# Optimization experiments

Measured on AMD Instinct MI355X. Metric: run time of the kernel, lower is better.

## Reference

```python
import jax, jax.numpy as jnp
import numpy as np

DIM = 192; D_STATE = 16; D_CONV = 4; EXPAND = 2
D_INNER = EXPAND * DIM          # 384
DT_RANK = -(-DIM // 16)         # ceil(192/16) = 12
BSZ, T, H, W = 1, 16, 64, 64


def setup_inputs() -> dict:
    key = jax.random.key(0)
    ks = jax.random.split(key, 10)
    s = 0.02
    return {
        "x": jax.random.normal(ks[0], (BSZ, DIM, T, H, W), jnp.float32),
        "ln1_g": jnp.ones((DIM,), jnp.float32),
        "ln1_b": jnp.zeros((DIM,), jnp.float32),
        "ln2_g": jnp.ones((DIM,), jnp.float32),
        "ln2_b": jnp.zeros((DIM,), jnp.float32),
        "W_in": jax.random.normal(ks[1], (2 * D_INNER, DIM), jnp.float32) * s,
        "conv_w": jax.random.normal(ks[2], (D_INNER, D_CONV), jnp.float32) * 0.3,
        "conv_b": jnp.zeros((D_INNER,), jnp.float32),
        "W_xp": jax.random.normal(ks[3], (DT_RANK + 2 * D_STATE, D_INNER), jnp.float32) * s,
        "W_dt": jax.random.normal(ks[4], (D_INNER, DT_RANK), jnp.float32) * 0.1,
        "b_dt": jax.random.normal(ks[5], (D_INNER,), jnp.float32) * 0.1 - 4.0,
        "A_log": jnp.log(jnp.broadcast_to(jnp.arange(1, D_STATE + 1, dtype=jnp.float32), (D_INNER, D_STATE))),
        "D": jnp.ones((D_INNER,), jnp.float32),
        "W_out": jax.random.normal(ks[6], (DIM, D_INNER), jnp.float32) * s,
    }


def _layer_norm(x, g, b, eps=1e-5):
    m = x.mean(-1, keepdims=True)
    v = ((x - m) ** 2).mean(-1, keepdims=True)
    return (x - m) * jax.lax.rsqrt(v + eps) * g + b


def _mamba(tokens, W_in, conv_w, conv_b, W_xp, W_dt, b_dt, A_log, D, W_out):
    B, L, _ = tokens.shape
    xz = tokens @ W_in.T                      # (B, L, 2*d_inner)
    xc, z = jnp.split(xz, 2, axis=-1)
    # causal depthwise conv1d along L
    xin = xc.transpose(0, 2, 1)               # (B, d_inner, L)
    xconv = jax.lax.conv_general_dilated(
        xin, conv_w[:, None, :], (1,), [(D_CONV - 1, 0)],
        dimension_numbers=("NCH", "OIH", "NCH"), feature_group_count=D_INNER)
    xconv = xconv + conv_b[None, :, None]
    xs = jax.nn.silu(xconv.transpose(0, 2, 1))  # (B, L, d_inner)
    x_dbl = xs @ W_xp.T                        # (B, L, dt_rank + 2*d_state)
    dt, Bm, Cm = jnp.split(x_dbl, [DT_RANK, DT_RANK + D_STATE], axis=-1)
    dt = jax.nn.softplus(dt @ W_dt.T + b_dt)   # (B, L, d_inner)
    A = -jnp.exp(A_log)                        # (d_inner, d_state)
    dA = jnp.exp(dt[..., None] * A)            # (B, L, d_inner, d_state)
    dBx = dt[..., None] * Bm[:, :, None, :] * xs[..., None]

    def step(h, inp):
        dA_t, dBx_t, C_t = inp
        h = dA_t * h + dBx_t                   # (B, d_inner, d_state)
        return h, jnp.einsum("bds,bs->bd", h, C_t)

    h0 = jnp.zeros((B, D_INNER, D_STATE), tokens.dtype)
    _, ys = jax.lax.scan(step, h0, (dA.transpose(1, 0, 2, 3),
                                    dBx.transpose(1, 0, 2, 3),
                                    Cm.transpose(1, 0, 2)))
    y = ys.transpose(1, 0, 2) + xs * D         # (B, L, d_inner)
    y = y * jax.nn.silu(z)
    return y @ W_out.T                          # (B, L, dim)


def reference(x, ln1_g, ln1_b, ln2_g, ln2_b, W_in, conv_w, conv_b,
              W_xp, W_dt, b_dt, A_log, D, W_out):
    B, C, T_, H_, W_ = x.shape
    Hs, Ws = H_ // 4, W_ // 4
    # avg_pool3d kernel=(1,4,4) stride=(1,4,4)
    x_ds = x.reshape(B, C, T_, Hs, 4, Ws, 4).mean((4, 6))
    tokens = x_ds.reshape(B, C, T_ * Hs * Ws).transpose(0, 2, 1)  # (B, L, C)
    y = _layer_norm(tokens, ln1_g, ln1_b)
    y = _mamba(y, W_in, conv_w, conv_b, W_xp, W_dt, b_dt, A_log, D, W_out)
    out = _layer_norm(tokens + y, ln2_g, ln2_b)                    # (B, L, C)
    out5 = out.transpose(0, 2, 1).reshape(B, C, T_, Hs, Ws)
    pooled = out5.mean((3, 4))                                     # (B, C, T)
    mag = jnp.abs(jnp.fft.rfft(pooled, axis=2))
    weight = jax.nn.sigmoid(mag[:, :, 1:8].mean(-1))               # (B, C)
    out5 = out5 * weight[:, :, None, None, None]
    up = jax.image.resize(out5, (B, C, T_, H_, W_), method="trilinear")
    return up * jax.nn.sigmoid(x)
```

## Files before the change

kernel.cpp:

```cpp
#include <hip/hip_runtime.h>
#include <math.h>

#define DIMC 192
#define DI   384
#define DS   16
#define LTOK 4096
#define NCH  128
#define CLEN 32
#define NLANE (DI*DS)
#define L2E  1.4426950408889634f
#define LN2  0.6931471805599453f

typedef __attribute__((ext_vector_type(8))) short    bf16x8;
typedef __attribute__((ext_vector_type(8))) unsigned short u16x8;
typedef __attribute__((ext_vector_type(4))) float    f32x4;

__device__ __forceinline__ float EXP2(float x) { return __builtin_amdgcn_exp2f(x); }
__device__ __forceinline__ float RCP(float x)  { return __builtin_amdgcn_rcpf(x); }
__device__ __forceinline__ float LOG2(float x) { return __builtin_amdgcn_logf(x); }

__device__ __forceinline__ float sigmoidf_(float x) { return RCP(1.f + EXP2(-x * L2E)); }
__device__ __forceinline__ float siluf_(float x)    { return x * RCP(1.f + EXP2(-x * L2E)); }
__device__ __forceinline__ unsigned short f2bf(float f) {
    unsigned int u = __float_as_uint(f);
    u += 0x7FFFu + ((u >> 16) & 1u);
    return (unsigned short)(u >> 16);
}
__device__ __forceinline__ float bf2f(unsigned short b) {
    return __uint_as_float(((unsigned int)b) << 16);
}

__global__ __launch_bounds__(256) void poolln_kernel(const float* __restrict__ x,
                                                     const float* __restrict__ g,
                                                     const float* __restrict__ bb,
                                                     const float* __restrict__ W_in,
                                                     const float* __restrict__ W_out,
                                                     const float* __restrict__ W_xp,
                                                     const float* __restrict__ A_log,
                                                     unsigned short* __restrict__ tokb,
                                                     unsigned short* __restrict__ ytok,
                                                     unsigned short* __restrict__ W_in_bf,
                                                     unsigned short* __restrict__ W_out_bf,
                                                     unsigned short* __restrict__ W_xp_pad,
                                                     float* __restrict__ A2pre,
                                                     float* __restrict__ pooled) {
    int blk = blockIdx.x;
    int tid = threadIdx.x;
    if (blk >= 256) {
        int id = (blk - 256) * 256 + tid;
        for (int i = id; i < 768 * 192; i += 8192) W_in_bf[i] = f2bf(W_in[i]);
        for (int i = id; i < 192 * 384; i += 8192) W_out_bf[i] = f2bf(W_out[i]);
        for (int i = id; i < 64 * 384; i += 8192) {
            int row = i / 384;
            W_xp_pad[i] = (row < 44) ? f2bf(W_xp[i]) : (unsigned short)0;
        }
        for (int i = id; i < NLANE; i += 8192) A2pre[i] = -expf(A_log[i]) * L2E;
        for (int i = id; i < 192 * 16; i += 8192) pooled[i] = 0.f;
        return;
    }
    int t = blk >> 4, hs = blk & 15;
    int grp = tid >> 4, ws = tid & 15;
    __shared__ float P[16 * 196];
    __shared__ float ms[16], rs[16];
    #pragma unroll
    for (int k = 0; k < 12; ++k) {
        int c = grp + (k << 4);
        const float* base = x + ((size_t)(c * 16 + t) * 64 + hs * 4) * 64 + ws * 4;
        float s = 0.f;
        #pragma unroll
        for (int i = 0; i < 4; ++i) {
            float4 v = *(const float4*)(base + i * 64);
            s += v.x + v.y + v.z + v.w;
        }
        P[ws * 196 + c] = s * 0.0625f;
    }
    __syncthreads();
    float s1 = 0.f, s2 = 0.f;
    #pragma unroll
    for (int k = 0; k < 12; ++k) {
        float v = P[grp * 196 + ws + 16 * k];
        s1 += v; s2 += v * v;
    }
    s1 += __shfl_xor(s1, 1); s2 += __shfl_xor(s2, 1);
    s1 += __shfl_xor(s1, 2); s2 += __shfl_xor(s2, 2);
    s1 += __shfl_xor(s1, 4); s2 += __shfl_xor(s2, 4);
    s1 += __shfl_xor(s1, 8); s2 += __shfl_xor(s2, 8);
    if (ws == 0) {
        float m = s1 * (1.f / 192.f);
        ms[grp] = m;
        rs[grp] = rsqrtf(s2 * (1.f / 192.f) - m * m + 1e-5f);
    }
    __syncthreads();
    int l0 = t * 256 + hs * 16;
    for (int e = tid; e < 16 * 192; e += 256) {
        int w2 = e / 192, c = e - w2 * 192;
        float v = P[w2 * 196 + c];
        float val = (v - ms[w2]) * rs[w2] * g[c] + bb[c];
        tokb[(size_t)(l0 + w2) * DIMC + c] = f2bf(v);
        ytok[(size_t)(l0 + w2) * DIMC + c] = f2bf(val);
    }
}

__global__ __launch_bounds__(256) void gemm_in(const unsigned short* __restrict__ A,
                                               const unsigned short* __restrict__ Wb,
                                               unsigned short* __restrict__ xcb,
                                               unsigned short* __restrict__ zsb) {
    constexpr int K = 192, KP = K + 8;
    __shared__ unsigned short As[64 * KP];
    __shared__ unsigned short Bs[64 * KP];
    int bm = blockIdx.y * 64;
    int bn = blockIdx.x * 64;
    int tid = threadIdx.x;
    int lane = tid & 63, w = tid >> 6;
    int wr = w >> 1, wc = w & 1;
    int r16 = lane & 15, h = lane >> 4;
    for (int c = tid; c < 64 * (K / 8); c += 256) {
        int row = c / (K / 8), col = (c % (K / 8)) * 8;
        *(u16x8*)&As[row * KP + col] = *(const u16x8*)(A + (size_t)(bm + row) * K + col);
        *(u16x8*)&Bs[row * KP + col] = *(const u16x8*)(Wb + (size_t)(bn + row) * K + col);
    }
    __syncthreads();
    f32x4 acc[2][2] = {};
    #pragma unroll
    for (int k0 = 0; k0 < K; k0 += 32) {
        bf16x8 a0 = *(const bf16x8*)&As[(wr * 32 + r16)      * KP + k0 + 8 * h];
        bf16x8 a1 = *(const bf16x8*)&As[(wr * 32 + 16 + r16) * KP + k0 + 8 * h];
        bf16x8 b0 = *(const bf16x8*)&Bs[(wc * 32 + r16)      * KP + k0 + 8 * h];
        bf16x8 b1 = *(const bf16x8*)&Bs[(wc * 32 + 16 + r16) * KP + k0 + 8 * h];
        acc[0][0] = __builtin_amdgcn_mfma_f32_16x16x32_bf16(a0, b0, acc[0][0], 0, 0, 0);
        acc[0][1] = __builtin_amdgcn_mfma_f32_16x16x32_bf16(a0, b1, acc[0][1], 0, 0, 0);
        acc[1][0] = __builtin_amdgcn_mfma_f32_16x16x32_bf16(a1, b0, acc[1][0], 0, 0, 0);
        acc[1][1] = __builtin_amdgcn_mfma_f32_16x16x32_bf16(a1, b1, acc[1][1], 0, 0, 0);
    }
    bool isz = (bn >= 384);
    #pragma unroll
    for (int fm = 0; fm < 2; ++fm)
        #pragma unroll
        for (int fn = 0; fn < 2; ++fn)
            #pragma unroll
            for (int i = 0; i < 4; ++i) {
                int r = bm + wr * 32 + fm * 16 + h * 4 + i;
                int cc = bn + wc * 32 + fn * 16 + r16;
                float v = acc[fm][fn][i];
                if (isz) zsb[(size_t)r * DI + (cc - 384)] = f2bf(siluf_(v));
                else     xcb[(size_t)r * DI + cc]         = f2bf(v);
            }
}

__global__ __launch_bounds__(256) void convxdbl(const unsigned short* __restrict__ xcb,
                                                const float* __restrict__ conv_w,
                                                const float* __restrict__ conv_b,
                                                const unsigned short* __restrict__ Wxp,
                                                unsigned short* __restrict__ xsb,
                                                float* __restrict__ x_dbl) {
    int l0 = blockIdx.x * 16;
    int tid = threadIdx.x;
    __shared__ unsigned short As[16 * 392];
    __shared__ float xd[16 * 64];
    for (int e = tid * 2; e < 16 * 384; e += 512) {
        int row = e / 384, d = e - row * 384;
        int l = l0 + row;
        float ax = conv_b[d], ay = conv_b[d + 1];
        #pragma unroll
        for (int k = 0; k < 4; ++k) {
            int ll = l - 3 + k;
            if (ll >= 0) {
                ushort2 u = *(const ushort2*)(xcb + (size_t)ll * DI + d);
                ax = fmaf(conv_w[d * 4 + k],       bf2f(u.x), ax);
                ay = fmaf(conv_w[(d + 1) * 4 + k], bf2f(u.y), ay);
            }
        }
        ushort2 b2;
        b2.x = f2bf(siluf_(ax));
        b2.y = f2bf(siluf_(ay));
        *(ushort2*)&As[row * 392 + d] = b2;
        *(ushort2*)(xsb + (size_t)l * 384 + d) = b2;
    }
    __syncthreads();
    int lane = tid & 63, w = tid >> 6;
    int r16 = lane & 15, hh = lane >> 4;
    f32x4 acc = {};
    #pragma unroll
    for (int k0 = 0; k0 < 384; k0 += 32) {
        bf16x8 a = *(const bf16x8*)&As[r16 * 392 + k0 + 8 * hh];
        bf16x8 b = *(const bf16x8*)(Wxp + (size_t)(w * 16 + r16) * 384 + k0 + 8 * hh);
        acc = __builtin_amdgcn_mfma_f32_16x16x32_bf16(a, b, acc, 0, 0, 0);
    }
    #pragma unroll
    for (int i = 0; i < 4; ++i) xd[(hh * 4 + i) * 64 + w * 16 + r16] = acc[i];
    __syncthreads();
    {
        int e = tid * 4;
        int row = e >> 6, col = e & 63;
        *(float4*)(x_dbl + (size_t)(l0 + row) * 64 + col) = *(const float4*)&xd[e];
    }
}

__global__ __launch_bounds__(256) void scan1(const float* __restrict__ x_dbl,
                                             const unsigned short* __restrict__ xsb,
                                             const float* __restrict__ W_dt,
                                             const float* __restrict__ b_dt,
                                             const float* __restrict__ A2pre,
                                             float* __restrict__ chA,
                                             float* __restrict__ chB,
                                             float* __restrict__ Dloc,
                                             unsigned short* __restrict__ yloc) {
    int tid = threadIdx.x;
    int dg = blockIdx.x;
    int c  = blockIdx.y;
    __shared__ float xdblS[CLEN * 48];
    __shared__ float wdtS[64 * 13];
    __shared__ float dtS[CLEN][64];
    __shared__ unsigned short xsS[CLEN][64];
    for (int i = tid; i < CLEN * 48; i += 256) {
        int row = i / 48, col = i - row * 48;
        xdblS[i] = x_dbl[(size_t)(c * CLEN + row) * 64 + col];
    }
    for (int i = tid; i < 768; i += 256) {
        int dl_ = i / 12, r = i - dl_ * 12;
        wdtS[dl_ * 13 + r] = W_dt[(size_t)dg * 768 + i];
    }
    for (int i = tid; i < CLEN * 64; i += 256) {
        int row = i >> 6, dl_ = i & 63;
        xsS[row][dl_] = xsb[(size_t)(c * CLEN + row) * 384 + dg * 64 + dl_];
    }
    __syncthreads();
    {
        int dl_ = tid & 63;
        float bd = b_dt[dg * 64 + dl_];
        #pragma unroll
        for (int i2 = 0; i2 < CLEN / 4; ++i2) {
            int row = (tid >> 6) + 4 * i2;
            float s = bd;
            #pragma unroll
            for (int r = 0; r < 12; ++r)
                s = fmaf(xdblS[row * 48 + r], wdtS[dl_ * 13 + r], s);
            dtS[row][dl_] = (s > 20.f) ? s : LOG2(1.f + EXP2(s * L2E)) * LN2;
        }
    }
    __syncthreads();
    int sq = tid & 3, dl = tid >> 2;
    int d = dg * 64 + dl;
    float4 a4 = *(const float4*)(A2pre + (size_t)d * DS + sq * 4);
    float A2[4] = {a4.x, a4.y, a4.z, a4.w};
    float h[4] = {};
    float dts = 0.f;
    #pragma unroll
    for (int i = 0; i < CLEN; ++i) {
        int l = c * CLEN + i;
        float dtv = dtS[i][dl];
        float xv  = bf2f(xsS[i][dl]);
        float dtx = dtv * xv;
        dts += dtv;
        float y = 0.f;
        #pragma unroll
        for (int u = 0; u < 4; ++u) {
            float a = EXP2(dtv * A2[u]);
            h[u] = fmaf(a, h[u], dtx * xdblS[i * 48 + 12 + sq * 4 + u]);
            y = fmaf(h[u], xdblS[i * 48 + 28 + sq * 4 + u], y);
        }
        y += __shfl_xor(y, 1);
        y += __shfl_xor(y, 2);
        if (sq == 0) {
            yloc[(size_t)l * DI + d] = f2bf(y);
            Dloc[(size_t)l * DI + d] = dts;
        }
    }
    size_t base = (size_t)c * NLANE + d * DS + sq * 4;
    float4 pa, pb;
    pa.x = EXP2(dts * A2[0]); pa.y = EXP2(dts * A2[1]);
    pa.z = EXP2(dts * A2[2]); pa.w = EXP2(dts * A2[3]);
    pb.x = h[0]; pb.y = h[1]; pb.z = h[2]; pb.w = h[3];
    *(float4*)&chA[base] = pa;
    *(float4*)&chB[base] = pb;
}

__global__ __launch_bounds__(256) void scan2p(const float* __restrict__ chA,
                                              const float* __restrict__ chB,
                                              float* __restrict__ hst) {
    int tid = threadIdx.x;
    int ll = tid & 31;
    int g  = tid >> 5;
    int lane = blockIdx.x * 32 + ll;
    float a[16], b[16];
    #pragma unroll
    for (int i = 0; i < 16; ++i) {
        int c = g * 16 + i;
        a[i] = chA[(size_t)c * NLANE + lane];
        b[i] = chB[(size_t)c * NLANE + lane];
    }
    float Ath = 1.f, Bth = 0.f;
    #pragma unroll
    for (int i = 0; i < 16; ++i) {
        Bth = fmaf(a[i], Bth, b[i]);
        Ath *= a[i];
    }
    __shared__ float sA[8][33], sB[8][33];
    sA[g][ll] = Ath; sB[g][ll] = Bth;
    __syncthreads();
    #pragma unroll
    for (int step = 1; step < 8; step <<= 1) {
        float pA = 1.f, pB = 0.f;
        if (g >= step) { pA = sA[g - step][ll]; pB = sB[g - step][ll]; }
        __syncthreads();
        if (g >= step) {
            float cA = sA[g][ll], cB = sB[g][ll];
            sA[g][ll] = cA * pA;
            sB[g][ll] = fmaf(cA, pB, cB);
        }
        __syncthreads();
    }
    float h = (g == 0) ? 0.f : sB[g - 1][ll];
    #pragma unroll
    for (int i = 0; i < 16; ++i) {
        int c = g * 16 + i;
        hst[(size_t)c * NLANE + lane] = h;
        h = fmaf(a[i], h, b[i]);
    }
}

__global__ __launch_bounds__(512) void gemmscanln(const float* __restrict__ hst,
                                                  const float* __restrict__ Dloc,
                                                  const float* __restrict__ x_dbl,
                                                  const float* __restrict__ A2pre,
                                                  const unsigned short* __restrict__ yloc,
                                                  const unsigned short* __restrict__ xsb,
                                                  const unsigned short* __restrict__ zsb,
                                                  const float* __restrict__ Dvec,
                                                  const unsigned short* __restrict__ Wb,
                                                  const unsigned short* __restrict__ tokb,
                                                  const float* __restrict__ g,
                                                  const float* __restrict__ bb,
                                                  float* __restrict__ o5,
                                                  float* __restrict__ pooled) {
    constexpr int K = 384, KT = 96, KP = KT + 8;
    __shared__ unsigned short ybufS[16 * 392];
    __shared__ char smem2[192 * KP * 2];
    unsigned short* Bs = (unsigned short*)smem2;
    float* P = (float*)smem2;
    __shared__ float hpS[2][16 * 17];
    __shared__ float A2S[2][16 * 17];
    __shared__ float CsS[256];
    __shared__ float ms[16], rs[16];
    int c = blockIdx.x;
    int c32 = c >> 1;
    int tid = threadIdx.x;
    int half = tid >> 8, t8 = tid & 255;
    int ll = t8 >> 4, sl = t8 & 15;
    if (tid < 256) CsS[tid] = x_dbl[(size_t)(c * 16 + (tid >> 4)) * 64 + 28 + (tid & 15)];
    int l = c * 16 + ll;
    for (int dgi = 0; dgi < 12; ++dgi) {
        int dg = dgi * 2 + half;
        hpS[half][ll * 17 + sl] = hst[(size_t)c32 * NLANE + dg * 256 + t8];
        A2S[half][ll * 17 + sl] = A2pre[(size_t)dg * 256 + t8];
        __syncthreads();
        int d = dg * 16 + sl;
        float Dl = Dloc[(size_t)l * DI + d];
        float y  = bf2f(yloc[(size_t)l * DI + d]);
        float xv = bf2f(xsb[(size_t)l * DI + d]);
        float zs = bf2f(zsb[(size_t)l * DI + d]);
        #pragma unroll
        for (int s = 0; s < 16; ++s) {
            float e = EXP2(A2S[half][sl * 17 + s] * Dl);
            y = fmaf(CsS[ll * 16 + s] * e, hpS[half][sl * 17 + s], y);
        }
        float val = (y + xv * Dvec[d]) * zs;
        ybufS[ll * 392 + d] = f2bf(val);
        __syncthreads();
    }
    int lane = tid & 63, w = tid >> 6;
    int r16 = lane & 15, hh = lane >> 4;
    f32x4 acc0 = {}, acc1 = {};
    for (int kt = 0; kt < K; kt += KT) {
        for (int cc2 = tid; cc2 < 192 * 12; cc2 += 512) {
            int row = cc2 / 12, col = (cc2 % 12) * 8;
            *(u16x8*)&Bs[row * KP + col] = *(const u16x8*)(Wb + (size_t)row * K + kt + col);
        }
        __syncthreads();
        #pragma unroll
        for (int k0 = 0; k0 < KT; k0 += 32) {
            bf16x8 a = *(const bf16x8*)&ybufS[r16 * 392 + kt + k0 + 8 * hh];
            bf16x8 b0 = *(const bf16x8*)&Bs[(w * 16 + r16) * KP + k0 + 8 * hh];
            acc0 = __builtin_amdgcn_mfma_f32_16x16x32_bf16(a, b0, acc0, 0, 0, 0);
            if (w < 4) {
                bf16x8 b1 = *(const bf16x8*)&Bs[((8 + w) * 16 + r16) * KP + k0 + 8 * hh];
                acc1 = __builtin_amdgcn_mfma_f32_16x16x32_bf16(a, b1, acc1, 0, 0, 0);
            }
        }
        __syncthreads();
    }
    for (int e = tid; e < 16 * 192; e += 512) {
        int row = e / 192, col = e - row * 192;
        P[row * 193 + col] = bf2f(tokb[(size_t)(c * 16 + row) * DIMC + col]);
    }
    __syncthreads();
    #pragma unroll
    for (int i = 0; i < 4; ++i)
        P[(hh * 4 + i) * 193 + w * 16 + r16] += acc0[i];
    if (w < 4)
        #pragma unroll
        for (int i = 0; i < 4; ++i)
            P[(hh * 4 + i) * 193 + (8 + w) * 16 + r16] += acc1[i];
    __syncthreads();
    {
        int tk = tid >> 5, q = tid & 31;
        float s1 = 0.f, s2 = 0.f;
        #pragma unroll
        for (int u = 0; u < 6; ++u) {
            float v = P[tk * 193 + q * 6 + u];
            s1 += v; s2 += v * v;
        }
        s1 += __shfl_xor(s1, 1);  s2 += __shfl_xor(s2, 1);
        s1 += __shfl_xor(s1, 2);  s2 += __shfl_xor(s2, 2);
        s1 += __shfl_xor(s1, 4);  s2 += __shfl_xor(s2, 4);
        s1 += __shfl_xor(s1, 8);  s2 += __shfl_xor(s2, 8);
        s1 += __shfl_xor(s1, 16); s2 += __shfl_xor(s2, 16);
        if (q == 0) {
            float m = s1 * (1.f / 192.f);
            ms[tk] = m;
            rs[tk] = rsqrtf(s2 * (1.f / 192.f) - m * m + 1e-5f);
        }
    }
    __syncthreads();
    int t = c >> 4;
    int sp0 = (c * 16) & 255;
    for (int e = tid; e < 16 * 192; e += 512) {
        int cch = e >> 4, row = e & 15;
        float val = (P[row * 193 + cch] - ms[row]) * rs[row] * g[cch] + bb[cch];
        o5[(size_t)cch * 4096 + t * 256 + sp0 + row] = val;
        float s = val;
        s += __shfl_xor(s, 1); s += __shfl_xor(s, 2);
        s += __shfl_xor(s, 4); s += __shfl_xor(s, 8);
        if (row == 0) atomicAdd(&pooled[cch * 16 + t], s);
    }
}

__global__ __launch_bounds__(256) void upfft(const float* __restrict__ o5,
                                             const float* __restrict__ pooled,
                                             const float* __restrict__ x,
                                             float* __restrict__ out) {
    int blk = blockIdx.x;
    int c = blk >> 4, t = blk & 15;
    int tid = threadIdx.x;
    __shared__ float pl[256];
    __shared__ float mag[8];
    __shared__ float wgt_s;
    pl[tid] = o5[(size_t)c * 4096 + t * 256 + tid];
    if (tid >= 1 && tid <= 7) {
        int k = tid;
        float re = 0.f, im = 0.f;
        for (int tt = 0; tt < 16; ++tt) {
            float pv = pooled[c * 16 + tt] * (1.f / 256.f);
            float ang = -0.39269908169872414f * (float)(k * tt);
            re = fmaf(pv, __cosf(ang), re);
            im = fmaf(pv, __sinf(ang), im);
        }
        mag[k] = sqrtf(re * re + im * im);
    }
    __syncthreads();
    if (tid == 0) {
        float m = 0.f;
        for (int k = 1; k <= 7; ++k) m += mag[k];
        wgt_s = sigmoidf_(m * (1.f / 7.f));
    }
    __syncthreads();
    float wc = wgt_s;
    size_t planeoff = (size_t)blk * 4096;
    #pragma unroll
    for (int p = 0; p < 4; ++p) {
        int px4 = p * 256 + tid;
        int k = px4 & 15;
        int hrow = px4 >> 4;
        float sh = hrow * 0.25f - 0.375f;
        int h0 = (int)floorf(sh); float fh = sh - (float)h0;
        int h0c = min(max(h0, 0), 15), h1c = min(max(h0 + 1, 0), 15);
        int cm = max(k - 1, 0), cp = min(k + 1, 15);
        float r0m = pl[h0c * 16 + cm], r00 = pl[h0c * 16 + k], r0p = pl[h0c * 16 + cp];
        float r1m = pl[h1c * 16 + cm], r10 = pl[h1c * 16 + k], r1p = pl[h1c * 16 + cp];
        float gh = 1.f - fh;
        float vm = r0m * gh + r1m * fh;
        float v0 = r00 * gh + r10 * fh;
        float vp = r0p * gh + r1p * fh;
        size_t off = planeoff + (size_t)px4 * 4;
        float4 xv = *(const float4*)(x + off);
        float4 o;
        o.x = (vm * 0.375f + v0 * 0.625f) * wc * sigmoidf_(xv.x);
        o.y = (vm * 0.125f + v0 * 0.875f) * wc * sigmoidf_(xv.y);
        o.z = (v0 * 0.875f + vp * 0.125f) * wc * sigmoidf_(xv.z);
        o.w = (v0 * 0.625f + vp * 0.375f) * wc * sigmoidf_(xv.w);
        *(float4*)(out + off) = o;
    }
}

extern "C" void kernel_launch(void* const* d_in, const int* in_sizes, int n_in,
                              void* d_out, int out_size, void* d_ws, size_t ws_size,
                              hipStream_t stream) {
    const float* x      = (const float*)d_in[0];
    const float* ln1_g  = (const float*)d_in[1];
    const float* ln1_b  = (const float*)d_in[2];
    const float* ln2_g  = (const float*)d_in[3];
    const float* ln2_b  = (const float*)d_in[4];
    const float* W_in   = (const float*)d_in[5];
    const float* conv_w = (const float*)d_in[6];
    const float* conv_b = (const float*)d_in[7];
    const float* W_xp   = (const float*)d_in[8];
    const float* W_dt   = (const float*)d_in[9];
    const float* b_dt   = (const float*)d_in[10];
    const float* A_log  = (const float*)d_in[11];
    const float* Dvec   = (const float*)d_in[12];
    const float* W_out  = (const float*)d_in[13];
    float* out = (float*)d_out;

    float* ws = (float*)d_ws;
    float* x_dbl  = ws;  ws += (size_t)LTOK * 64;
    float* chA    = ws;  ws += (size_t)NLANE * NCH;
    float* chB    = ws;  ws += (size_t)NLANE * NCH;
    float* hst    = ws;  ws += (size_t)NLANE * NCH;
    float* Dloc   = ws;  ws += (size_t)LTOK * DI;
    float* o5     = ws;  ws += (size_t)DIMC * LTOK;
    float* A2pre  = ws;  ws += NLANE;
    float* pooled = ws;  ws += 192 * 16;
    unsigned short* tokb     = (unsigned short*)ws;  ws += (size_t)LTOK * DIMC / 2;
    unsigned short* ytok     = (unsigned short*)ws;  ws += (size_t)LTOK * DIMC / 2;
    unsigned short* yloc     = (unsigned short*)ws;  ws += (size_t)LTOK * DI / 2;
    unsigned short* xsb      = (unsigned short*)ws;  ws += (size_t)LTOK * DI / 2;
    unsigned short* xcb      = (unsigned short*)ws;  ws += (size_t)LTOK * DI / 2;
    unsigned short* zsb      = (unsigned short*)ws;  ws += (size_t)LTOK * DI / 2;
    unsigned short* W_in_bf  = (unsigned short*)ws;  ws += (size_t)768 * 192 / 2;
    unsigned short* W_out_bf = (unsigned short*)ws;  ws += (size_t)192 * 384 / 2;
    unsigned short* W_xp_pad = (unsigned short*)ws;  ws += (size_t)64 * 384 / 2;

    poolln_kernel<<<288, 256, 0, stream>>>(x, ln1_g, ln1_b, W_in, W_out, W_xp, A_log,
                                           tokb, ytok, W_in_bf, W_out_bf, W_xp_pad, A2pre, pooled);
    gemm_in<<<dim3(12, 64), 256, 0, stream>>>(ytok, W_in_bf, xcb, zsb);
    convxdbl<<<256, 256, 0, stream>>>(xcb, conv_w, conv_b, W_xp_pad, xsb, x_dbl);
    scan1<<<dim3(6, NCH), 256, 0, stream>>>(x_dbl, xsb, W_dt, b_dt, A2pre, chA, chB, Dloc, yloc);
    scan2p<<<NLANE / 32, 256, 0, stream>>>(chA, chB, hst);
    gemmscanln<<<256, 512, 0, stream>>>(hst, Dloc, x_dbl, A2pre, yloc, xsb, zsb, Dvec,
                                        W_out_bf, tokb, ln2_g, ln2_b, o5, pooled);
    upfft<<<3072, 256, 0, stream>>>(o5, pooled, x, out);
}
```

Baseline: 114.1 us.

## Split fused scan-fix/out-proj/LN kernel into separate scan fixup and GEMM+LN kernels

Replaces the single fused kernel (256 blocks of 512 threads running a serial 12-step scan fixup, then the output projection and layer norm) with two kernels. The scan fixup now runs as a 24x256 grid with one 16x16 tile per block and writes bf16 results back into yloc in place. The GEMM+LN kernel uses 512 blocks of 8 tokens each, with the MFMA A tile zero-padded to 16 rows, so half of every MFMA is wasted. The aim is more parallelism and occupancy, at the cost of an extra launch and a global round trip for the y buffer.

```diff
diff --git a/kernel.cpp b/kernel.cpp
--- a/kernel.cpp
+++ b/kernel.cpp
@@ -319,88 +319,93 @@
     }
 }
 
-__global__ __launch_bounds__(512) void gemmscanln(const float* __restrict__ hst,
-                                                  const float* __restrict__ Dloc,
-                                                  const float* __restrict__ x_dbl,
-                                                  const float* __restrict__ A2pre,
-                                                  const unsigned short* __restrict__ yloc,
-                                                  const unsigned short* __restrict__ xsb,
-                                                  const unsigned short* __restrict__ zsb,
-                                                  const float* __restrict__ Dvec,
-                                                  const unsigned short* __restrict__ Wb,
-                                                  const unsigned short* __restrict__ tokb,
-                                                  const float* __restrict__ g,
-                                                  const float* __restrict__ bb,
-                                                  float* __restrict__ o5,
-                                                  float* __restrict__ pooled) {
+__global__ __launch_bounds__(256) void scan3fix(const float* __restrict__ hst,
+                                                const float* __restrict__ Dloc,
+                                                const float* __restrict__ x_dbl,
+                                                const float* __restrict__ A2pre,
+                                                const unsigned short* __restrict__ xsb,
+                                                const unsigned short* __restrict__ zsb,
+                                                const float* __restrict__ Dvec,
+                                                unsigned short* __restrict__ ybuf) {
+    int dg = blockIdx.x;
+    int c  = blockIdx.y;
+    int tid = threadIdx.x;
+    int ll = tid >> 4, dl = tid & 15;
+    int d = dg * 16 + dl;
+    int l = c * 16 + ll;
+    __shared__ float hpS[16][17];
+    __shared__ float A2S[16][17];
+    __shared__ float CsS[256];
+    {
+        int dd = tid >> 4, ss = tid & 15;
+        hpS[dd][ss] = hst[(size_t)(c >> 1) * NLANE + dg * 256 + tid];
+        A2S[dd][ss] = A2pre[(size_t)dg * 256 + tid];
+        CsS[tid]    = x_dbl[(size_t)(c * 16 + dd) * 64 + 28 + ss];
+    }
+    __syncthreads();
+    float Dl = Dloc[(size_t)l * DI + d];
+    float y  = bf2f(ybuf[(size_t)l * DI + d]);
+    float xv = bf2f(xsb[(size_t)l * DI + d]);
+    float zs = bf2f(zsb[(size_t)l * DI + d]);
+    #pragma unroll
+    for (int s = 0; s < 16; ++s) {
+        float e = EXP2(A2S[dl][s] * Dl);
+        y = fmaf(CsS[ll * 16 + s] * e, hpS[dl][s], y);
+    }
+    float val = (y + xv * Dvec[d]) * zs;
+    ybuf[(size_t)l * DI + d] = f2bf(val);
+}
+
+__global__ __launch_bounds__(256) void gemmln(const unsigned short* __restrict__ A,
+                                              const unsigned short* __restrict__ Wb,
+                                              const unsigned short* __restrict__ tokb,
+                                              const float* __restrict__ g,
+                                              const float* __restrict__ bb,
+                                              float* __restrict__ o5,
+                                              float* __restrict__ pooled) {
     constexpr int K = 384, KT = 96, KP = KT + 8;
-    __shared__ unsigned short ybufS[16 * 392];
-    __shared__ char smem2[192 * KP * 2];
-    unsigned short* Bs = (unsigned short*)smem2;
-    float* P = (float*)smem2;
-    __shared__ float hpS[2][16 * 17];
-    __shared__ float A2S[2][16 * 17];
-    __shared__ float CsS[256];
-    __shared__ float ms[16], rs[16];
-    int c = blockIdx.x;
-    int c32 = c >> 1;
-    int tid = threadIdx.x;
-    int half = tid >> 8, t8 = tid & 255;
-    int ll = t8 >> 4, sl = t8 & 15;
-    if (tid < 256) CsS[tid] = x_dbl[(size_t)(c * 16 + (tid >> 4)) * 64 + 28 + (tid & 15)];
-    int l = c * 16 + ll;
-    for (int dgi = 0; dgi < 12; ++dgi) {
-        int dg = dgi * 2 + half;
-        hpS[half][ll * 17 + sl] = hst[(size_t)c32 * NLANE + dg * 256 + t8];
-        A2S[half][ll * 17 + sl] = A2pre[(size_t)dg * 256 + t8];
-        __syncthreads();
-        int d = dg * 16 + sl;
-        float Dl = Dloc[(size_t)l * DI + d];
-        float y  = bf2f(yloc[(size_t)l * DI + d]);
-        float xv = bf2f(xsb[(size_t)l * DI + d]);
-        float zs = bf2f(zsb[(size_t)l * DI + d]);
-        #pragma unroll
-        for (int s = 0; s < 16; ++s) {
-            float e = EXP2(A2S[half][sl * 17 + s] * Dl);
-            y = fmaf(CsS[ll * 16 + s] * e, hpS[half][sl * 17 + s], y);
-        }
-        float val = (y + xv * Dvec[d]) * zs;
-        ybufS[ll * 392 + d] = f2bf(val);
-        __syncthreads();
-    }
+    __shared__ unsigned short ybS[16 * 392];
+    __shared__ unsigned short Bs[192 * KP];
+    __shared__ float P[8 * 193];
+    __shared__ float ms[8], rs[8];
+    int l0 = blockIdx.x * 8;
+    int tid = threadIdx.x;
+    for (int e = tid; e < 8 * 48; e += 256) {
+        int row = e / 48, col = (e % 48) * 8;
+        *(u16x8*)&ybS[row * 392 + col] = *(const u16x8*)(A + (size_t)(l0 + row) * DI + col);
+    }
+    for (int e = tid; e < 8 * 392; e += 256) ybS[8 * 392 + e] = 0;
     int lane = tid & 63, w = tid >> 6;
     int r16 = lane & 15, hh = lane >> 4;
-    f32x4 acc0 = {}, acc1 = {};
+    f32x4 acc[3] = {};
     for (int kt = 0; kt < K; kt += KT) {
-        for (int cc2 = tid; cc2 < 192 * 12; cc2 += 512) {
-            int row = cc2 / 12, col = (cc2 % 12) * 8;
+        for (int cc = tid; cc < 192 * 12; cc += 256) {
+            int row = cc / 12, col = (cc % 12) * 8;
             *(u16x8*)&Bs[row * KP + col] = *(const u16x8*)(Wb + (size_t)row * K + kt + col);
         }
         __syncthreads();
         #pragma unroll
         for (int k0 = 0; k0 < KT; k0 += 32) {
-            bf16x8 a = *(const bf16x8*)&ybufS[r16 * 392 + kt + k0 + 8 * hh];
-            bf16x8 b0 = *(const bf16x8*)&Bs[(w * 16 + r16) * KP + k0 + 8 * hh];
-            acc0 = __builtin_amdgcn_mfma_f32_16x16x32_bf16(a, b0, acc0, 0, 0, 0);
-            if (w < 4) {
-                bf16x8 b1 = *(const bf16x8*)&Bs[((8 + w) * 16 + r16) * KP + k0 + 8 * hh];
-                acc1 = __builtin_amdgcn_mfma_f32_16x16x32_bf16(a, b1, acc1, 0, 0, 0);
+            bf16x8 a = *(const bf16x8*)&ybS[r16 * 392 + kt + k0 + 8 * hh];
+            #pragma unroll
+            for (int j = 0; j < 3; ++j) {
+                bf16x8 bfrag = *(const bf16x8*)&Bs[((w * 3 + j) * 16 + r16) * KP + k0 + 8 * hh];
+                acc[j] = __builtin_amdgcn_mfma_f32_16x16x32_bf16(a, bfrag, acc[j], 0, 0, 0);
             }
         }
         __syncthreads();
     }
-    for (int e = tid; e < 16 * 192; e += 512) {
+    for (int e = tid; e < 8 * 192; e += 256) {
         int row = e / 192, col = e - row * 192;
-        P[row * 193 + col] = bf2f(tokb[(size_t)(c * 16 + row) * DIMC + col]);
-    }
-    __syncthreads();
-    #pragma unroll
-    for (int i = 0; i < 4; ++i)
-        P[(hh * 4 + i) * 193 + w * 16 + r16] += acc0[i];
-    if (w < 4)
-        #pragma unroll
-        for (int i = 0; i < 4; ++i)
-            P[(hh * 4 + i) * 193 + (8 + w) * 16 + r16] += acc1[i];
+        P[row * 193 + col] = bf2f(tokb[(size_t)(l0 + row) * DIMC + col]);
+    }
+    __syncthreads();
+    if (hh < 2)
+        #pragma unroll
+        for (int j = 0; j < 3; ++j)
+            #pragma unroll
+            for (int i = 0; i < 4; ++i)
+                P[(hh * 4 + i) * 193 + (w * 3 + j) * 16 + r16] += acc[j][i];
     __syncthreads();
     {
         int tk = tid >> 5, q = tid & 31;
@@ -422,15 +427,14 @@
         }
     }
     __syncthreads();
-    int t = c >> 4;
-    int sp0 = (c * 16) & 255;
-    for (int e = tid; e < 16 * 192; e += 512) {
-        int cch = e >> 4, row = e & 15;
+    int t = l0 >> 8;
+    int sp0 = l0 & 255;
+    for (int e = tid; e < 8 * 192; e += 256) {
+        int cch = e >> 3, row = e & 7;
         float val = (P[row * 193 + cch] - ms[row]) * rs[row] * g[cch] + bb[cch];
         o5[(size_t)cch * 4096 + t * 256 + sp0 + row] = val;
         float s = val;
-        s += __shfl_xor(s, 1); s += __shfl_xor(s, 2);
-        s += __shfl_xor(s, 4); s += __shfl_xor(s, 8);
+        s += __shfl_xor(s, 1); s += __shfl_xor(s, 2); s += __shfl_xor(s, 4);
         if (row == 0) atomicAdd(&pooled[cch * 16 + t], s);
     }
 }
@@ -536,7 +540,7 @@
     convxdbl<<<256, 256, 0, stream>>>(xcb, conv_w, conv_b, W_xp_pad, xsb, x_dbl);
     scan1<<<dim3(6, NCH), 256, 0, stream>>>(x_dbl, xsb, W_dt, b_dt, A2pre, chA, chB, Dloc, yloc);
     scan2p<<<NLANE / 32, 256, 0, stream>>>(chA, chB, hst);
-    gemmscanln<<<256, 512, 0, stream>>>(hst, Dloc, x_dbl, A2pre, yloc, xsb, zsb, Dvec,
-                                        W_out_bf, tokb, ln2_g, ln2_b, o5, pooled);
+    scan3fix<<<dim3(24, 256), 256, 0, stream>>>(hst, Dloc, x_dbl, A2pre, xsb, zsb, Dvec, yloc);
+    gemmln<<<512, 256, 0, stream>>>(yloc, W_out_bf, tokb, ln2_g, ln2_b, o5, pooled);
     upfft<<<3072, 256, 0, stream>>>(o5, pooled, x, out);
 }
```

Result: slower. 134.6 us (+18.0%).
